# Kernel tuning notes

Measured on AMD Instinct MI355X. Metric: run time of the kernel, lower is better.

## Reference

```python
import jax, jax.numpy as jnp
import numpy as np

B, T, D = 32, 1024, 384
T_OUT = 4096  # static padded output length (= target_len for every batch element)


def setup_inputs() -> dict:
    key = jax.random.key(0)
    k1, k2 = jax.random.split(key)
    x = jax.random.normal(k1, (B, T, D), dtype=jnp.float32)
    durations = jax.random.randint(k2, (B, T), 0, 8, dtype=jnp.int32)
    # constant target length -> torch pads/truncates every row to T_OUT,
    # and max over batch is T_OUT, so output is [B, T_OUT, D].
    target_len = jnp.full((B,), T_OUT, dtype=jnp.int32)
    return {"x": x, "durations": durations, "target_len": target_len}


def reference(x, durations, target_len):
    # x: [B, T, D]; durations: [B, T] int; target_len: [B] int.
    # Ragged repeat-expansion expressed as cumulative-duration searchsorted + gather.
    Bx, Tx, Dx = x.shape
    dur = jnp.maximum(durations, 0)
    ends = jnp.cumsum(dur, axis=1)              # [B, T] exclusive-end frame index per token
    total = ends[:, -1]                          # [B] total expanded length per batch row
    pos = jnp.arange(T_OUT, dtype=ends.dtype)    # [T_OUT] output frame positions
    # token index owning each output frame: number of ends <= pos
    idx = jax.vmap(lambda e: jnp.searchsorted(e, pos, side="right"))(ends)  # [B, T_OUT]
    idx = jnp.clip(idx, 0, Tx - 1)
    out = jnp.take_along_axis(x, idx[..., None], axis=1)  # [B, T_OUT, D]
    # frames past min(total_expansion, target_len) are zero padding (truncate + pad semantics)
    limit = jnp.minimum(total, target_len.astype(total.dtype))  # [B]
    valid = pos[None, :] < limit[:, None]                        # [B, T_OUT]
    return jnp.where(valid[..., None], out, jnp.zeros((), x.dtype))
```

## Files before the change

### kernel.cpp

```cpp
#include <hip/hip_runtime.h>


#define BB 32
#define TT 1024
#define DD 384
#define TOUT 4096
#define D4 (DD / 4)
#define N4 (TOUT * D4)
#define EPB 3072
#define ROWS_PB 32
#define KPT 12

typedef float v4f __attribute__((ext_vector_type(4)));

__global__ __launch_bounds__(256) void lr_scan(
    const int4* __restrict__ dur4,
    const int* __restrict__ target_len,
    int4* __restrict__ ends4,
    int* __restrict__ limit)
{
    __shared__ int sums[256];
    const int b = blockIdx.x;
    const int q = threadIdx.x;

    int4 d = dur4[b * 256 + q];
    const int d0 = d.x > 0 ? d.x : 0;
    const int d1 = d.y > 0 ? d.y : 0;
    const int d2 = d.z > 0 ? d.z : 0;
    const int d3 = d.w > 0 ? d.w : 0;
    const int e0 = d0, e1 = e0 + d1, e2 = e1 + d2, e3 = e2 + d3;
    sums[q] = e3;
    __syncthreads();

    #pragma unroll
    for (int off = 1; off < 256; off <<= 1) {
        int u = (q >= off) ? sums[q - off] : 0;
        __syncthreads();
        sums[q] += u;
        __syncthreads();
    }
    const int base = sums[q] - e3;
    ends4[b * 256 + q] = make_int4(base + e0, base + e1, base + e2, base + e3);

    if (q == 255) {
        const int total = base + e3;
        const int tl = target_len[b];
        limit[b] = total < tl ? total : tl;
    }
}

__global__ __launch_bounds__(256) void lr_gather(
    const v4f* __restrict__ x,
    const int4* __restrict__ ends4,
    const int* __restrict__ limit,
    v4f* __restrict__ out)
{
    __shared__ int s_ends[TT];
    __shared__ int s_trow[ROWS_PB];
    const int b = blockIdx.y;
    const int tid = threadIdx.x;
    const int base0 = blockIdx.x * EPB;
    const int p0 = blockIdx.x * ROWS_PB;

    ((int4*)s_ends)[tid] = ends4[b * 256 + tid];
    const int lim = limit[b];
    __syncthreads();

    if (tid < ROWS_PB) {
        const int p = p0 + tid;
        int lo = 0;
        #pragma unroll
        for (int s = 512; s > 0; s >>= 1) {
            lo += (s_ends[lo + s - 1] <= p) ? s : 0;
        }
        s_trow[tid] = lo;
    }
    __syncthreads();

    const v4f* __restrict__ x_b = x + b * TT * D4;
    v4f* __restrict__ out_b = out + b * N4;

    int pp[KPT], cc[KPT], tt[KPT];
    v4f v[KPT];
    #pragma unroll
    for (int k = 0; k < KPT; ++k) {
        const int i = base0 + k * 256 + tid;
        const int p = i / D4;
        pp[k] = p;
        cc[k] = i - p * D4;
        tt[k] = s_trow[p - p0];
    }
    #pragma unroll
    for (int k = 0; k < KPT; ++k) {
        v[k] = x_b[tt[k] * D4 + cc[k]];
    }
    #pragma unroll
    for (int k = 0; k < KPT; ++k) {
        if (pp[k] >= lim) v[k] = (v4f)(0.f);
        __builtin_nontemporal_store(v[k], out_b + base0 + k * 256 + tid);
    }
}

extern "C" void kernel_launch(void* const* d_in, const int* in_sizes, int n_in,
                              void* d_out, int out_size, void* d_ws, size_t ws_size,
                              hipStream_t stream) {
    const float* x        = (const float*)d_in[0];
    const int* durations  = (const int*)d_in[1];
    const int* target_len = (const int*)d_in[2];
    float* out            = (float*)d_out;

    int* limit = (int*)d_ws;
    int* ends  = (int*)d_ws + 64;

    lr_scan<<<BB, 256, 0, stream>>>((const int4*)durations, target_len,
                                    (int4*)ends, limit);

    dim3 grid(N4 / EPB, BB);
    lr_gather<<<grid, 256, 0, stream>>>((const v4f*)x, (const int4*)ends,
                                        limit, (v4f*)out);
}
```

Measured before the change: 243.1 us.

## Fuse duration scan into gather kernel using wave shuffle prefix sum

```diff
diff --git a/kernel.cpp b/kernel.cpp
--- a/kernel.cpp
+++ b/kernel.cpp
@@ -3,9 +3,8 @@
 
 #define BB 32
 #define TT 1024
-#define DD 384
 #define TOUT 4096
-#define D4 (DD / 4)
+#define D4 96
 #define N4 (TOUT * D4)
 #define EPB 3072
 #define ROWS_PB 32
@@ -13,57 +12,48 @@
 
 typedef float v4f __attribute__((ext_vector_type(4)));
 
-__global__ __launch_bounds__(256) void lr_scan(
+__global__ __launch_bounds__(256) void lr_fused(
     const int4* __restrict__ dur4,
     const int* __restrict__ target_len,
-    int4* __restrict__ ends4,
-    int* __restrict__ limit)
+    const v4f* __restrict__ x,
+    v4f* __restrict__ out)
 {
-    __shared__ int sums[256];
-    const int b = blockIdx.x;
-    const int q = threadIdx.x;
+    __shared__ int s_ends[TT];
+    __shared__ int s_wsum[4];
+    __shared__ int s_trow[ROWS_PB];
+    const int b = blockIdx.y;
+    const int tid = threadIdx.x;
+    const int lane = tid & 63;
+    const int wave = tid >> 6;
+    const int base0 = blockIdx.x * EPB;
+    const int p0 = blockIdx.x * ROWS_PB;
 
-    int4 d = dur4[b * 256 + q];
+    const int tl = target_len[b];
+
+    int4 d = dur4[b * 256 + tid];
     const int d0 = d.x > 0 ? d.x : 0;
     const int d1 = d.y > 0 ? d.y : 0;
     const int d2 = d.z > 0 ? d.z : 0;
     const int d3 = d.w > 0 ? d.w : 0;
     const int e0 = d0, e1 = e0 + d1, e2 = e1 + d2, e3 = e2 + d3;
-    sums[q] = e3;
+
+    int v = e3;
+    #pragma unroll
+    for (int off = 1; off < 64; off <<= 1) {
+        int u = __shfl_up(v, off, 64);
+        if (lane >= off) v += u;
+    }
+    if (lane == 63) s_wsum[wave] = v;
     __syncthreads();
 
+    int wbase = 0;
     #pragma unroll
-    for (int off = 1; off < 256; off <<= 1) {
-        int u = (q >= off) ? sums[q - off] : 0;
-        __syncthreads();
-        sums[q] += u;
-        __syncthreads();
-    }
-    const int base = sums[q] - e3;
-    ends4[b * 256 + q] = make_int4(base + e0, base + e1, base + e2, base + e3);
+    for (int w = 0; w < 3; ++w) wbase += (w < wave) ? s_wsum[w] : 0;
+    const int total = s_wsum[0] + s_wsum[1] + s_wsum[2] + s_wsum[3];
+    const int lim = total < tl ? total : tl;
 
-    if (q == 255) {
-        const int total = base + e3;
-        const int tl = target_len[b];
-        limit[b] = total < tl ? total : tl;
-    }
-}
-
-__global__ __launch_bounds__(256) void lr_gather(
-    const v4f* __restrict__ x,
-    const int4* __restrict__ ends4,
-    const int* __restrict__ limit,
-    v4f* __restrict__ out)
-{
-    __shared__ int s_ends[TT];
-    __shared__ int s_trow[ROWS_PB];
-    const int b = blockIdx.y;
-    const int tid = threadIdx.x;
-    const int base0 = blockIdx.x * EPB;
-    const int p0 = blockIdx.x * ROWS_PB;
-
-    ((int4*)s_ends)[tid] = ends4[b * 256 + tid];
-    const int lim = limit[b];
+    const int base = wbase + v - e3;
+    ((int4*)s_ends)[tid] = make_int4(base + e0, base + e1, base + e2, base + e3);
     __syncthreads();
 
     if (tid < ROWS_PB) {
@@ -81,7 +71,7 @@
     v4f* __restrict__ out_b = out + b * N4;
 
     int pp[KPT], cc[KPT], tt[KPT];
-    v4f v[KPT];
+    v4f vv[KPT];
     #pragma unroll
     for (int k = 0; k < KPT; ++k) {
         const int i = base0 + k * 256 + tid;
@@ -92,12 +82,12 @@
     }
     #pragma unroll
     for (int k = 0; k < KPT; ++k) {
-        v[k] = x_b[tt[k] * D4 + cc[k]];
+        vv[k] = x_b[tt[k] * D4 + cc[k]];
     }
     #pragma unroll
     for (int k = 0; k < KPT; ++k) {
-        if (pp[k] >= lim) v[k] = (v4f)(0.f);
-        __builtin_nontemporal_store(v[k], out_b + base0 + k * 256 + tid);
+        if (pp[k] >= lim) vv[k] = (v4f)(0.f);
+        __builtin_nontemporal_store(vv[k], out_b + base0 + k * 256 + tid);
     }
 }
 
@@ -109,13 +99,7 @@
     const int* target_len = (const int*)d_in[2];
     float* out            = (float*)d_out;
 
-    int* limit = (int*)d_ws;
-    int* ends  = (int*)d_ws + 64;
-
-    lr_scan<<<BB, 256, 0, stream>>>((const int4*)durations, target_len,
-                                    (int4*)ends, limit);
-
     dim3 grid(N4 / EPB, BB);
-    lr_gather<<<grid, 256, 0, stream>>>((const v4f*)x, (const int4*)ends,
-                                        limit, (v4f*)out);
+    lr_fused<<<grid, 256, 0, stream>>>((const int4*)durations, target_len,
+                                       (const v4f*)x, (v4f*)out);
 }
```

Result: no change. 240.4 us (-1.1%).
